# Performance work log

Measured on AMD Instinct MI355X. Metric: run time of the kernel, lower is better.

The kernel has to match this reference:

```python
import jax, jax.numpy as jnp
import numpy as np

EMB = 1024
NUM_HEAD = 16
HEAD_DIM = EMB // NUM_HEAD


def setup_inputs() -> dict:
    key = jax.random.key(0)
    ks = jax.random.split(key, 7)
    bound = 1.0 / np.sqrt(EMB)  # kaiming_uniform-ish scale
    inp = {
        "source_emb": jax.random.normal(ks[0], (2, 2048, EMB), jnp.float32),
        "target_emb": jax.random.normal(ks[1], (2, 2048, EMB), jnp.float32),
        "Wq": jax.random.uniform(ks[2], (EMB, EMB), jnp.float32, -bound, bound),
        "Wk": jax.random.uniform(ks[3], (EMB, EMB), jnp.float32, -bound, bound),
        "Wv": jax.random.uniform(ks[4], (EMB, EMB), jnp.float32, -bound, bound),
        "Wo": jax.random.uniform(ks[5], (EMB, EMB), jnp.float32, -bound, bound),
        "bo": jnp.zeros((EMB,), jnp.float32),
    }
    return inp


def reference(source_emb, target_emb, Wq, Wk, Wv, Wo, bo):
    B, T, E = target_emb.shape
    S = source_emb.shape[1]
    H, D = NUM_HEAD, HEAD_DIM
    # projections (torch Linear: x @ W.T), split into heads
    q = (target_emb @ Wq.T).reshape(B, T, H, D)
    k = (source_emb @ Wk.T).reshape(B, S, H, D)
    v = (source_emb @ Wv.T).reshape(B, S, H, D)
    scale = 1.0 / jnp.sqrt(jnp.asarray(D, q.dtype))
    # scores: [B, H, T, S] (materialized, as in the original bmm path)
    scores = jnp.einsum("bthd,bshd->bhts", q * scale, k)
    attn = jax.nn.softmax(scores, axis=-1)  # dropout p=0.0 in eval
    # context: [B, T, H, D] -> [B, T, E]
    ctx = jnp.einsum("bhts,bshd->bthd", attn, v).reshape(B, T, E)
    out = ctx @ Wo.T + bo
    # batch_size > 1 branch: return full per-head attention
    return out, attn
```

## Files before the change

kernel.cpp:

```cpp
#include <hip/hip_runtime.h>
#include <cstdint>


typedef __attribute__((ext_vector_type(8))) short short8;
typedef __attribute__((ext_vector_type(4))) short short4v;
typedef __attribute__((ext_vector_type(4))) float floatx4;

__device__ __forceinline__ short f2bf(float f) {
    union { float f; unsigned u; } c; c.f = f;
    unsigned r = c.u + 0x7FFFu + ((c.u >> 16) & 1u);
    return (short)(r >> 16);
}

__device__ __forceinline__ void async_copy16(void* lds, const void* g) {
    __builtin_amdgcn_global_load_lds((const __attribute__((address_space(1))) void*)g,
                                     (__attribute__((address_space(3))) void*)lds,
                                     16, 0, 0);
}

__device__ __forceinline__ void barrier_lds_only() {
    asm volatile("s_waitcnt lgkmcnt(0)" ::: "memory");
    __builtin_amdgcn_sched_barrier(0);
    __builtin_amdgcn_s_barrier();
    __builtin_amdgcn_sched_barrier(0);
    asm volatile("" ::: "memory");
}

__global__ __launch_bounds__(256) void cast_all(
    const float* __restrict__ a0, const float* __restrict__ a1,
    const float* __restrict__ a2, const float* __restrict__ a3,
    const float* __restrict__ a4, const float* __restrict__ a5,
    short* __restrict__ o0, short* __restrict__ o1, short* __restrict__ o2,
    short* __restrict__ o3, short* __restrict__ o4, short* __restrict__ o5)
{
    long i = ((long)blockIdx.x * 256 + threadIdx.x) * 8;
    const float* s; short* d; long off;
    if      (i <  4194304) { s = a0; d = o0; off = 0; }
    else if (i <  8388608) { s = a1; d = o1; off = 4194304; }
    else if (i <  9437184) { s = a2; d = o2; off = 8388608; }
    else if (i < 10485760) { s = a3; d = o3; off = 9437184; }
    else if (i < 11534336) { s = a4; d = o4; off = 10485760; }
    else                   { s = a5; d = o5; off = 11534336; }
    long j = i - off;
    float4 x0 = *(const float4*)(s + j);
    float4 x1 = *(const float4*)(s + j + 4);
    short8 r;
    r[0] = f2bf(x0.x); r[1] = f2bf(x0.y); r[2] = f2bf(x0.z); r[3] = f2bf(x0.w);
    r[4] = f2bf(x1.x); r[5] = f2bf(x1.y); r[6] = f2bf(x1.z); r[7] = f2bf(x1.w);
    *(short8*)(d + j) = r;
}

__global__ __launch_bounds__(256) void proj_qkv(
    const short* __restrict__ xt, const short* __restrict__ xs,
    const short* __restrict__ wq, const short* __restrict__ wk,
    const short* __restrict__ wv,
    short* __restrict__ qb, short* __restrict__ kb, short* __restrict__ vtb)
{
    __shared__ __align__(16) short sA[128 * 32];
    __shared__ __align__(16) short sB[128 * 32];
    const int bid = blockIdx.x;
    const short *A, *Bm; short *outp; int mode; float scale; int bx, by;
    if (bid < 256)      { A = xt; Bm = wq; outp = qb;  mode = 0; scale = 0.125f;
                          bx = bid & 7;  by = bid >> 3; }
    else if (bid < 512) { int t = bid - 256; A = xs; Bm = wk; outp = kb;
                          mode = 0; scale = 1.0f; bx = t & 7;  by = t >> 3; }
    else                { int t = bid - 512; A = wv; Bm = xs; outp = vtb;
                          mode = 1; scale = 1.0f; bx = t & 31; by = t >> 5; }
    const int m0 = by * 128, n0 = bx * 128;
    const int tid = threadIdx.x;
    const int ln = tid & 15, qd = (tid & 63) >> 4, w = tid >> 6;
    const int wm = (w >> 1) * 64, wn = (w & 1) * 64;
    floatx4 acc[4][4] = {};

    for (int k0 = 0; k0 < 1024; k0 += 32) {
#pragma unroll
        for (int u = 0; u < 2; ++u) {
            int f = tid + u * 256;
            int row = f >> 2, ch = (f & 3) * 8;
            async_copy16(&sA[f * 8], A + (long)(m0 + row) * 1024 + k0 + ch);
            async_copy16(&sB[f * 8], Bm + (long)(n0 + row) * 1024 + k0 + ch);
        }
        __syncthreads();
        short8 a8[4], b8[4];
#pragma unroll
        for (int i = 0; i < 4; ++i)
            a8[i] = *(const short8*)&sA[(wm + i * 16 + ln) * 32 + qd * 8];
#pragma unroll
        for (int j = 0; j < 4; ++j)
            b8[j] = *(const short8*)&sB[(wn + j * 16 + ln) * 32 + qd * 8];
#pragma unroll
        for (int i = 0; i < 4; ++i)
#pragma unroll
            for (int j = 0; j < 4; ++j)
                acc[i][j] = __builtin_amdgcn_mfma_f32_16x16x32_bf16(
                    a8[i], b8[j], acc[i][j], 0, 0, 0);
        __syncthreads();
    }

#pragma unroll
    for (int i = 0; i < 4; ++i)
#pragma unroll
        for (int j = 0; j < 4; ++j)
#pragma unroll
            for (int r = 0; r < 4; ++r) {
                int gm = m0 + wm + i * 16 + qd * 4 + r;
                int gn = n0 + wn + j * 16 + ln;
                float val = acc[i][j][r];
                if (mode == 0) {
                    int bb = gm >> 11, t = gm & 2047, hh = gn >> 6, d = gn & 63;
                    outp[((((long)(bb * 16 + hh) << 11) | t) << 6) | d] =
                        f2bf(val * scale);
                } else {
                    int hh = gm >> 6, d = gm & 63, bb = gn >> 11, s = gn & 2047;
                    outp[(((long)((bb * 16 + hh) * 64 + d)) << 11) | s] = f2bf(val);
                }
            }
}

template<int MODE>
__global__ __launch_bounds__(256) void gemm_bt(
    const short* __restrict__ A, const short* __restrict__ Bm,
    void* __restrict__ outp, const float* __restrict__ bias,
    int N, int K, int lda, int ldb, float scale)
{
    __shared__ __align__(16) short sA[128 * 32];
    __shared__ __align__(16) short sB[128 * 32];
    const int m0 = blockIdx.y * 128, n0 = blockIdx.x * 128;
    const int tid = threadIdx.x;
    const int ln = tid & 15, qd = (tid & 63) >> 4, w = tid >> 6;
    const int wm = (w >> 1) * 64, wn = (w & 1) * 64;
    floatx4 acc[4][4] = {};

    for (int k0 = 0; k0 < K; k0 += 32) {
#pragma unroll
        for (int u = 0; u < 2; ++u) {
            int f = tid + u * 256;
            int row = f >> 2, ch = (f & 3) * 8;
            async_copy16(&sA[f * 8], A + (long)(m0 + row) * lda + k0 + ch);
            async_copy16(&sB[f * 8], Bm + (long)(n0 + row) * ldb + k0 + ch);
        }
        __syncthreads();
        short8 a8[4], b8[4];
#pragma unroll
        for (int i = 0; i < 4; ++i)
            a8[i] = *(const short8*)&sA[(wm + i * 16 + ln) * 32 + qd * 8];
#pragma unroll
        for (int j = 0; j < 4; ++j)
            b8[j] = *(const short8*)&sB[(wn + j * 16 + ln) * 32 + qd * 8];
#pragma unroll
        for (int i = 0; i < 4; ++i)
#pragma unroll
            for (int j = 0; j < 4; ++j)
                acc[i][j] = __builtin_amdgcn_mfma_f32_16x16x32_bf16(
                    a8[i], b8[j], acc[i][j], 0, 0, 0);
        __syncthreads();
    }

#pragma unroll
    for (int i = 0; i < 4; ++i)
#pragma unroll
        for (int j = 0; j < 4; ++j)
#pragma unroll
            for (int r = 0; r < 4; ++r) {
                int gm = m0 + wm + i * 16 + qd * 4 + r;
                int gn = n0 + wn + j * 16 + ln;
                ((float*)outp)[(long)gm * N + gn] = acc[i][j][r] + bias[gn];
            }
}

__global__ __launch_bounds__(256) void fused_attn(
    const short* __restrict__ qb, const short* __restrict__ kb,
    const short* __restrict__ vtb, float* __restrict__ attn,
    short* __restrict__ ctx)
{
    const int bx = blockIdx.x;
    const int bh = bx & 31, mq = bx >> 5;
    const int b = bh >> 4, h = bh & 15;
    const int tid = threadIdx.x;
    const int ln = tid & 15, qd = (tid & 63) >> 4, w = tid >> 6;
    const int wt = (w >> 1) * 32;
    const int ws = (w & 1) * 64;

    __shared__ __align__(16) short sP[2][8192];
    __shared__ float rpart[2][64];
    __shared__ float rinv[64];

    const short* qbase = qb + ((long)bh * 2048 + mq * 64) * 64;
    const short* kbase = kb + (long)bh * 2048 * 64;
    const short* vbase = vtb + (long)bh * 64 * 2048;
    float* abase = attn + ((long)bh * 2048 + mq * 64) * 2048;

    short8 a8q[2][2];
#pragma unroll
    for (int j = 0; j < 2; ++j)
#pragma unroll
        for (int ks = 0; ks < 2; ++ks)
            a8q[j][ks] = *(const short8*)(qbase + (wt + j * 16 + ln) * 64
                                          + ks * 32 + qd * 8);

    float sumP[2] = {};
    for (int s0 = 0; s0 < 2048; s0 += 128) {
        floatx4 acc[4][2] = {};
#pragma unroll
        for (int i = 0; i < 4; ++i) {
            const short* kp = kbase + (long)(s0 + ws + i * 16 + ln) * 64 + qd * 8;
            short8 bk0 = *(const short8*)kp;
            short8 bk1 = *(const short8*)(kp + 32);
#pragma unroll
            for (int j = 0; j < 2; ++j) {
                acc[i][j] = __builtin_amdgcn_mfma_f32_16x16x32_bf16(
                    bk0, a8q[j][0], acc[i][j], 0, 0, 0);
                acc[i][j] = __builtin_amdgcn_mfma_f32_16x16x32_bf16(
                    bk1, a8q[j][1], acc[i][j], 0, 0, 0);
            }
        }
#pragma unroll
        for (int i = 0; i < 4; ++i)
#pragma unroll
            for (int j = 0; j < 2; ++j)
#pragma unroll
                for (int r = 0; r < 4; ++r)
                    sumP[j] += __expf(acc[i][j][r]);
    }
#pragma unroll
    for (int j = 0; j < 2; ++j) {
        float v = sumP[j];
        v += __shfl_xor(v, 16);
        v += __shfl_xor(v, 32);
        if ((tid & 48) == 0) rpart[w & 1][wt + j * 16 + ln] = v;
    }
    __syncthreads();
    if (tid < 64) rinv[tid] = 1.0f / (rpart[0][tid] + rpart[1][tid]);
    __syncthreads();
    float invP[2];
#pragma unroll
    for (int j = 0; j < 2; ++j)
        invP[j] = rinv[wt + j * 16 + ln];

    floatx4 accO[4] = {};
    int nb = 0;
    for (int s0 = 0; s0 < 2048; s0 += 128, nb ^= 1) {
        floatx4 acc[4][2] = {};
#pragma unroll
        for (int i = 0; i < 4; ++i) {
            const short* kp = kbase + (long)(s0 + ws + i * 16 + ln) * 64 + qd * 8;
            short8 bk0 = *(const short8*)kp;
            short8 bk1 = *(const short8*)(kp + 32);
#pragma unroll
            for (int j = 0; j < 2; ++j) {
                acc[i][j] = __builtin_amdgcn_mfma_f32_16x16x32_bf16(
                    bk0, a8q[j][0], acc[i][j], 0, 0, 0);
                acc[i][j] = __builtin_amdgcn_mfma_f32_16x16x32_bf16(
                    bk1, a8q[j][1], acc[i][j], 0, 0, 0);
            }
        }
#pragma unroll
        for (int i = 0; i < 4; ++i) {
            const int sb  = ws + i * 16 + qd * 4;
            const int grp = sb >> 3;
            const int sub = sb & 7;
#pragma unroll
            for (int j = 0; j < 2; ++j) {
                const int t = wt + j * 16 + ln;
                floatx4 p4;
#pragma unroll
                for (int r = 0; r < 4; ++r)
                    p4[r] = __expf(acc[i][j][r]) * invP[j];
                short4v c4;
#pragma unroll
                for (int r = 0; r < 4; ++r) c4[r] = f2bf(p4[r]);
                *(short4v*)&sP[nb][(grp * 64 + t) * 8 + sub] = c4;
                __builtin_nontemporal_store(
                    p4, (floatx4*)(abase + (long)t * 2048 + s0 + sb));
            }
        }
        barrier_lds_only();
#pragma unroll
        for (int ks = 0; ks < 4; ++ks) {
            short8 a0 = *(const short8*)&sP[nb][((ks * 4 + qd) * 64 + w * 16 + ln) * 8];
#pragma unroll
            for (int j = 0; j < 4; ++j) {
                short8 bv = *(const short8*)(vbase + (long)(j * 16 + ln) * 2048
                                             + s0 + ks * 32 + qd * 8);
                accO[j] = __builtin_amdgcn_mfma_f32_16x16x32_bf16(
                    a0, bv, accO[j], 0, 0, 0);
            }
        }
    }

#pragma unroll
    for (int j = 0; j < 4; ++j)
#pragma unroll
        for (int r = 0; r < 4; ++r) {
            int t = mq * 64 + w * 16 + qd * 4 + r;
            int d = j * 16 + ln;
            ctx[((long)(b * 2048 + t)) * 1024 + h * 64 + d] =
                f2bf(accO[j][r]);
        }
}

extern "C" void kernel_launch(void* const* d_in, const int* in_sizes, int n_in,
                              void* d_out, int out_size, void* d_ws, size_t ws_size,
                              hipStream_t stream)
{
    const float* src = (const float*)d_in[0];
    const float* tgt = (const float*)d_in[1];
    const float* Wq  = (const float*)d_in[2];
    const float* Wk  = (const float*)d_in[3];
    const float* Wv  = (const float*)d_in[4];
    const float* Wo  = (const float*)d_in[5];
    const float* bo  = (const float*)d_in[6];
    float* out  = (float*)d_out;
    float* attn = out + 4194304;

    char* ws = (char*)d_ws;
    short* xt  = (short*)(ws);
    short* xs  = (short*)(ws + (8L  << 20));
    short* wq  = (short*)(ws + (16L << 20));
    short* wk  = (short*)(ws + (18L << 20));
    short* wv  = (short*)(ws + (20L << 20));
    short* wo  = (short*)(ws + (22L << 20));
    short* qb  = (short*)(ws + (24L << 20));
    short* kb  = (short*)(ws + (32L << 20));
    short* vtb = (short*)(ws + (40L << 20));
    short* ctx = (short*)(ws);

    cast_all<<<6144, 256, 0, stream>>>(tgt, src, Wq, Wk, Wv, Wo,
                                       xt, xs, wq, wk, wv, wo);
    proj_qkv<<<768, 256, 0, stream>>>(xt, xs, wq, wk, wv, qb, kb, vtb);
    fused_attn<<<1024, 256, 0, stream>>>(qb, kb, vtb, attn, ctx);
    gemm_bt<3><<<dim3(8, 32, 1), 256, 0, stream>>>(ctx, wo, out, bo,
                                          1024, 1024, 1024, 1024, 1.0f);
}
```

Before: 827.0 us.

## Stage fp32 probabilities in swizzled LDS for coalesced attn stores

Each wave used to write the fp32 attention probabilities straight to global memory in a scattered 16-byte pattern. Now the probabilities go into a single XOR-swizzled fp32 LDS tile, are read back row-contiguously, and are stored to global in coalesced 512-byte rows. The bf16 conversion for the PV MFMA moves to the read side and uses packed v_cvt_pk_bf16_f32. The double buffer is dropped, so a second barrier per iteration is needed, and LDS traffic per iteration grows.

```diff
diff --git a/kernel.cpp b/kernel.cpp
--- a/kernel.cpp
+++ b/kernel.cpp
@@ -3,13 +3,21 @@
 
 
 typedef __attribute__((ext_vector_type(8))) short short8;
-typedef __attribute__((ext_vector_type(4))) short short4v;
 typedef __attribute__((ext_vector_type(4))) float floatx4;
 
 __device__ __forceinline__ short f2bf(float f) {
     union { float f; unsigned u; } c; c.f = f;
     unsigned r = c.u + 0x7FFFu + ((c.u >> 16) & 1u);
     return (short)(r >> 16);
+}
+
+__device__ __forceinline__ short8 pack8(floatx4 lo, floatx4 hi) {
+    union { short8 s; unsigned u[4]; } r;
+    asm("v_cvt_pk_bf16_f32 %0, %1, %2" : "=v"(r.u[0]) : "v"(lo[0]), "v"(lo[1]));
+    asm("v_cvt_pk_bf16_f32 %0, %1, %2" : "=v"(r.u[1]) : "v"(lo[2]), "v"(lo[3]));
+    asm("v_cvt_pk_bf16_f32 %0, %1, %2" : "=v"(r.u[2]) : "v"(hi[0]), "v"(hi[1]));
+    asm("v_cvt_pk_bf16_f32 %0, %1, %2" : "=v"(r.u[3]) : "v"(hi[2]), "v"(hi[3]));
+    return r.s;
 }
 
 __device__ __forceinline__ void async_copy16(void* lds, const void* g) {
@@ -181,7 +189,7 @@
     const int wt = (w >> 1) * 32;
     const int ws = (w & 1) * 64;
 
-    __shared__ __align__(16) short sP[2][8192];
+    __shared__ __align__(16) float sPf[64 * 128];
     __shared__ float rpart[2][64];
     __shared__ float rinv[64];
 
@@ -238,8 +246,7 @@
         invP[j] = rinv[wt + j * 16 + ln];
 
     floatx4 accO[4] = {};
-    int nb = 0;
-    for (int s0 = 0; s0 < 2048; s0 += 128, nb ^= 1) {
+    for (int s0 = 0; s0 < 2048; s0 += 128) {
         floatx4 acc[4][2] = {};
 #pragma unroll
         for (int i = 0; i < 4; ++i) {
@@ -256,9 +263,7 @@
         }
 #pragma unroll
         for (int i = 0; i < 4; ++i) {
-            const int sb  = ws + i * 16 + qd * 4;
-            const int grp = sb >> 3;
-            const int sub = sb & 7;
+            const int sb = ws + i * 16 + qd * 4;
 #pragma unroll
             for (int j = 0; j < 2; ++j) {
                 const int t = wt + j * 16 + ln;
@@ -266,18 +271,28 @@
 #pragma unroll
                 for (int r = 0; r < 4; ++r)
                     p4[r] = __expf(acc[i][j][r]) * invP[j];
-                short4v c4;
-#pragma unroll
-                for (int r = 0; r < 4; ++r) c4[r] = f2bf(p4[r]);
-                *(short4v*)&sP[nb][(grp * 64 + t) * 8 + sub] = c4;
-                __builtin_nontemporal_store(
-                    p4, (floatx4*)(abase + (long)t * 2048 + s0 + sb));
+                *(floatx4*)((char*)sPf + t * 512 + ((sb * 4) ^ ((t & 7) << 4))) = p4;
             }
         }
         barrier_lds_only();
 #pragma unroll
+        for (int u = 0; u < 8; ++u) {
+            int f = u * 256 + tid;
+            int row = f >> 5, c16 = f & 31;
+            floatx4 v = *(const floatx4*)((const char*)sPf + row * 512
+                                          + ((c16 * 16) ^ ((row & 7) << 4)));
+            __builtin_nontemporal_store(
+                v, (floatx4*)(abase + (long)row * 2048 + s0 + c16 * 4));
+        }
+        const int tr = w * 16 + ln;
+#pragma unroll
         for (int ks = 0; ks < 4; ++ks) {
-            short8 a0 = *(const short8*)&sP[nb][((ks * 4 + qd) * 64 + w * 16 + ln) * 8];
+            const int c = ks * 128 + qd * 32;
+            floatx4 f0 = *(const floatx4*)((const char*)sPf + tr * 512
+                                           + (c ^ ((tr & 7) << 4)));
+            floatx4 f1 = *(const floatx4*)((const char*)sPf + tr * 512
+                                           + ((c + 16) ^ ((tr & 7) << 4)));
+            short8 a0 = pack8(f0, f1);
 #pragma unroll
             for (int j = 0; j < 4; ++j) {
                 short8 bv = *(const short8*)(vbase + (long)(j * 16 + ln) * 2048
@@ -286,6 +301,7 @@
                     a0, bv, accO[j], 0, 0, 0);
             }
         }
+        barrier_lds_only();
     }
 
 #pragma unroll
```

Measured after the change: 846.9 us. 2.4% more time.
